# Optimization experiments

Measured on AMD Instinct MI355X. Metric: run time of the kernel, lower is better.

## Reference

```python
import jax, jax.numpy as jnp
from jax import lax
import numpy as np


def conv4d(x, w, b, pad):
    """4D conv (stride 1) as a sum of 3D convs over the first-spatial-dim kernel taps.
    x: [B, Cin, T, D, H, W]; w: [Cout, Cin, Kt, Kd, Kh, Kw]; same pad on all dims."""
    B, Cin, T, D, H, W = x.shape
    Cout, _, Kt = w.shape[:3]
    xp = jnp.pad(x, ((0, 0), (0, 0), (pad, pad), (0, 0), (0, 0), (0, 0)))
    Tout = T + 2 * pad - Kt + 1
    acc = None
    for k in range(Kt):  # loop over kernel taps (<=3), not data dims
        xs = xp[:, :, k:k + Tout]                      # [B,Cin,Tout,D,H,W]
        xs = xs.transpose(0, 2, 1, 3, 4, 5).reshape(B * Tout, Cin, D, H, W)
        y = lax.conv_general_dilated(
            xs, w[:, :, k], (1, 1, 1), [(pad, pad)] * 3,
            dimension_numbers=('NCDHW', 'OIDHW', 'NCDHW'))
        acc = y if acc is None else acc + y
    Do, Ho, Wo = acc.shape[2:]
    out = acc.reshape(B, Tout, Cout, Do, Ho, Wo).transpose(0, 2, 1, 3, 4, 5)
    return out + b[None, :, None, None, None, None]


def tconv4d_k2s2(x, w, b):
    """4D transposed conv, kernel=2, stride=2, pad=0 (non-overlapping blocks).
    x: [B,Cin,T,D,H,W]; w: [Cin,Cout,2,2,2,2] (PyTorch ConvTranspose layout)."""
    B, Cin, T, D, H, W = x.shape
    Cout = w.shape[1]
    y = jnp.einsum('bcijkl,copqrs->boipjqkrls', x, w)
    y = y.reshape(B, Cout, 2 * T, 2 * D, 2 * H, 2 * W)
    return y + b[None, :, None, None, None, None]


def setup_inputs() -> dict:
    key = jax.random.key(0)
    ks = jax.random.split(key, 10)
    Cin, Cout = 64, 32
    x1 = jax.random.normal(ks[0], (2, Cin, 8, 8, 8, 8), dtype=jnp.float32)
    x2 = jax.random.normal(ks[1], (2, Cin // 2, 16, 16, 16, 16), dtype=jnp.float32)
    def w(k, shape, fan_in):
        return jax.random.normal(k, shape, dtype=jnp.float32) / np.float32(np.sqrt(fan_in))
    up_w = w(ks[2], (Cin, Cin // 2, 2, 2, 2, 2), Cin * 16)
    up_b = w(ks[3], (Cin // 2,), Cin * 16)
    w1 = w(ks[4], (Cout, Cin, 3, 3, 3, 3), Cin * 81)
    b1 = w(ks[5], (Cout,), Cin * 81)
    w2 = w(ks[6], (Cout, Cout, 3, 3, 3, 3), Cout * 81)
    b2 = w(ks[7], (Cout,), Cout * 81)
    w3 = w(ks[8], (Cout, Cin, 1, 1, 1, 1), Cin)
    b3 = w(ks[9], (Cout,), Cin)
    return {'x1': x1, 'x2': x2, 'up_w': up_w, 'up_b': up_b,
            'w1': w1, 'b1': b1, 'w2': w2, 'b2': b2, 'w3': w3, 'b3': b3}


def reference(x1, x2, up_w, up_b, w1, b1, w2, b2, w3, b3):
    x1u = tconv4d_k2s2(x1, up_w, up_b)              # [B, Cin//2, 16,16,16,16]
    xc = jnp.concatenate([x2, x1u], axis=1)          # [B, Cin, 16,16,16,16]
    Y = jax.nn.relu(conv4d(xc, w1, b1, 1))
    Y = conv4d(Y, w2, b2, 1)
    sc = conv4d(xc, w3, b3, 0)                       # 1x1 residual projection
    return jax.nn.relu(Y + sc)
```

## Files before the change

### kernel.cpp

```cpp
#include <hip/hip_runtime.h>

typedef unsigned short u16;
typedef __attribute__((ext_vector_type(8))) short short8;
typedef __attribute__((ext_vector_type(4))) float f32x4;

#define XCB_OFF  0
#define Y1B_OFF  8388608
#define W1P_OFF  12582912
#define W2P_OFF  12748800
#define W3P_OFF  12831744
#define UPWP_OFF 12833792
#define X1T_OFF  12866560

__device__ __forceinline__ u16 f2bf(float v) {
    unsigned u = __builtin_bit_cast(unsigned, v);
    u += 0x7FFFu + ((u >> 16) & 1u);
    return (u16)(u >> 16);
}

__device__ __forceinline__ f32x4 MFMA(short8 a, short8 b, f32x4 c) {
    return __builtin_amdgcn_mfma_f32_16x16x32_bf16(a, b, c, 0, 0, 0);
}

__device__ __forceinline__ void decode_bid(int bid, int& b, int& t, int& d, int& h0) {
    int xcd = bid & 7, loc = bid >> 3;
    int hB = loc & 1;
    d = (loc >> 1) & 15;
    int tsub = (loc >> 5) & 1;
    b = loc >> 6;
    t = xcd * 2 + tsub;
    h0 = hB * 8;
}

__global__ __launch_bounds__(256) void setup(const float* __restrict__ w1,
                                             const float* __restrict__ w2,
                                             const float* __restrict__ w3,
                                             const float* __restrict__ upw,
                                             const float* __restrict__ x1,
                                             const float* __restrict__ x2,
                                             u16* __restrict__ ws) {
    __shared__ u16 lds[256 * 66];
    int bid = blockIdx.x;
    int tid = threadIdx.x;
    if (bid < 1108) {
        int idx = bid * 256 + tid;
        if (idx < 165888) {
            int j = idx & 7, lane = (idx >> 3) & 63, rest = idx >> 9;
            int half = rest & 1, chunk = (rest >> 1) & 1, tap = rest >> 2;
            int co = half * 16 + (lane & 15), ci = chunk * 32 + (lane >> 4) * 8 + j;
            ws[W1P_OFF + idx] = f2bf(w1[(co * 64 + ci) * 81 + tap]);
        } else if (idx < 165888 + 82944) {
            int i2 = idx - 165888;
            int j = i2 & 7, lane = (i2 >> 3) & 63, rest = i2 >> 9;
            int half = rest & 1, tap = rest >> 1;
            int co = half * 16 + (lane & 15), ci = (lane >> 4) * 8 + j;
            ws[W2P_OFF + i2] = f2bf(w2[(co * 32 + ci) * 81 + tap]);
        } else if (idx < 165888 + 82944 + 2048) {
            int i3 = idx - (165888 + 82944);
            int j = i3 & 7, lane = (i3 >> 3) & 63, rest = i3 >> 9;
            int half = rest & 1, chunk = rest >> 1;
            int co = half * 16 + (lane & 15), ci = chunk * 32 + (lane >> 4) * 8 + j;
            ws[W3P_OFF + i3] = f2bf(w3[co * 64 + ci]);
        } else if (idx < 250880 + 32768) {
            int i4 = idx - 250880;
            int j = i4 & 7, lane = (i4 >> 3) & 63, rest = i4 >> 9;
            int half = rest & 1, chunk = (rest >> 1) & 1, tap = rest >> 2;
            int co = half * 16 + (lane & 15), ci = chunk * 32 + (lane >> 4) * 8 + j;
            ws[UPWP_OFF + i4] = f2bf(upw[(ci * 32 + co) * 16 + tap]);
        }
    } else if (bid < 1620) {
        int lb = bid - 1108;
        int b = lb >> 8;
        int pos_base = (lb & 255) * 256;
        u16* xcb = ws + XCB_OFF;
        #pragma unroll
        for (int c = 0; c < 32; ++c) {
            lds[tid * 40 + c] = f2bf(x2[((b * 32 + c) << 16) + pos_base + tid]);
        }
        __syncthreads();
        #pragma unroll
        for (int k = 0; k < 4; ++k) {
            int f = k * 256 + tid;
            int u = f & 3, pos = f >> 2;
            uint4 v = *(const uint4*)(lds + pos * 40 + u * 8);
            *(uint4*)(xcb + (size_t)((b << 16) + pos_base + pos) * 64 + u * 8) = v;
        }
    } else {
        int lb = bid - 1620;
        int b = lb >> 4;
        int pos_base = (lb & 15) * 256;
        u16* x1t = ws + X1T_OFF;
        #pragma unroll
        for (int c = 0; c < 64; ++c) {
            lds[tid * 66 + c] = f2bf(x1[((b * 64 + c) << 12) + pos_base + tid]);
        }
        __syncthreads();
        #pragma unroll
        for (int k = 0; k < 64; ++k) {
            int f = k * 256 + tid;
            int ci = f & 63, pos = f >> 6;
            x1t[(size_t)((b << 12) + pos_base + pos) * 64 + ci] = lds[pos * 66 + ci];
        }
    }
}

__global__ __launch_bounds__(256) void xc_up_mfma(const u16* __restrict__ x1t,
                                                  const u16* __restrict__ upwp,
                                                  const float* __restrict__ up_b,
                                                  u16* __restrict__ xcb) {
    int tid = threadIdx.x;
    int wv = tid >> 6, lane = tid & 63;
    int q = lane >> 4, m = lane & 15;
    int wid = blockIdx.x * 4 + wv;
    int j = wid & 63, tap = (wid >> 6) & 15, b = wid >> 10;

    f32x4 acc[4][2];
    {
        float4 bi0 = ((const float4*)up_b)[q];
        float4 bi1 = ((const float4*)up_b)[4 + q];
        #pragma unroll
        for (int g = 0; g < 4; ++g) {
            acc[g][0] = (f32x4){bi0.x, bi0.y, bi0.z, bi0.w};
            acc[g][1] = (f32x4){bi1.x, bi1.y, bi1.z, bi1.w};
        }
    }

    const short8* wv8 = (const short8*)upwp;
    const u16* xb = x1t + (size_t)((b << 12) + (j << 6) + m) * 64;
    #pragma unroll
    for (int chunk = 0; chunk < 2; ++chunk) {
        short8 a0 = wv8[((tap * 2 + chunk) * 2 + 0) * 64 + lane];
        short8 a1 = wv8[((tap * 2 + chunk) * 2 + 1) * 64 + lane];
        #pragma unroll
        for (int g = 0; g < 4; ++g) {
            short8 bf = *(const short8*)(xb + (size_t)(g * 16) * 64 + chunk * 32 + q * 8);
            acc[g][0] = MFMA(a0, bf, acc[g][0]);
            acc[g][1] = MFMA(a1, bf, acc[g][1]);
        }
    }

    int it = j >> 3, id = j & 7;
    int pt = tap >> 3, pd = (tap >> 2) & 1, ph = (tap >> 1) & 1, pw = tap & 1;
    int oT = 2 * it + pt, oD = 2 * id + pd, oW = 2 * (m & 7) + pw;
    #pragma unroll
    for (int g = 0; g < 4; ++g) {
        int ih = g * 2 + (m >> 3);
        int opos = oT * 4096 + oD * 256 + (2 * ih + ph) * 16 + oW;
        u16* op = xcb + (size_t)((b << 16) + opos) * 64 + 32 + q * 4;
        #pragma unroll
        for (int half = 0; half < 2; ++half) {
            f32x4 v = acc[g][half];
            uint2 o;
            o.x = (unsigned)f2bf(v.x) | ((unsigned)f2bf(v.y) << 16);
            o.y = (unsigned)f2bf(v.z) | ((unsigned)f2bf(v.w) << 16);
            *(uint2*)(op + half * 16) = o;
        }
    }
}

__global__ __launch_bounds__(256, 4) void conv1_mfma(const u16* __restrict__ xcb,
                                                     const u16* __restrict__ w1p,
                                                     const float* __restrict__ b1,
                                                     u16* __restrict__ y1b) {
    __shared__ u16 lds[11520];
    int tid = threadIdx.x;
    int lane = tid & 63, wv = tid >> 6;
    int q = lane >> 4, m = lane & 15;
    int c = wv & 1, rg = wv >> 1;
    int b, t, d, h0;
    decode_bid(blockIdx.x, b, t, d, h0);
    int rot = (blockIdx.x * 5) % 9;

    int lofs[6], gofs[6];
    bool st[6], inr[6];
    #pragma unroll
    for (int k = 0; k < 6; ++k) {
        int ui = tid + k * 256;
        int u = ui & 7, p = (ui >> 3) % 18, hh = ui / 144;
        int gh = h0 - 1 + hh, gw = p - 1;
        st[k] = ui < 1440;
        inr[k] = st[k] && ((unsigned)gh < 16u) && ((unsigned)gw < 16u);
        gofs[k] = (gh * 16 + gw) * 64 + u * 8;
        lofs[k] = hh * 1152 + p * 64 + ((u ^ (p & 7)) * 8);
    }

    f32x4 acc[4][2];
    if (c == 0) {
        float4 bi0 = ((const float4*)b1)[q];
        float4 bi1 = ((const float4*)b1)[4 + q];
        #pragma unroll
        for (int i = 0; i < 4; ++i) {
            acc[i][0] = (f32x4){bi0.x, bi0.y, bi0.z, bi0.w};
            acc[i][1] = (f32x4){bi1.x, bi1.y, bi1.z, bi1.w};
        }
    } else {
        #pragma unroll
        for (int i = 0; i < 4; ++i) {
            acc[i][0] = (f32x4){0.f, 0.f, 0.f, 0.f};
            acc[i][1] = (f32x4){0.f, 0.f, 0.f, 0.f};
        }
    }
    const short8* w1v = (const short8*)w1p;

    uint4 rP[6];
    auto load_plane = [&](int ktd) {
        int kt = ktd / 3, kd = ktd - kt * 3;
        int tt = t + kt - 1, dd = d + kd - 1;
        bool pv = ((unsigned)tt < 16u) && ((unsigned)dd < 16u);
        const u16* src = xcb + (size_t)(((b * 16 + tt) * 16 + dd)) * 16384;
        #pragma unroll
        for (int k = 0; k < 6; ++k) {
            uint4 v = {0, 0, 0, 0};
            if (pv && inr[k]) v = *(const uint4*)(src + gofs[k]);
            rP[k] = v;
        }
    };
    auto write_plane = [&]() {
        #pragma unroll
        for (int k = 0; k < 6; ++k)
            if (st[k]) *(uint4*)(lds + lofs[k]) = rP[k];
    };

    load_plane(rot);
    for (int s = 0; s < 9; ++s) {
        int ktd = rot + s; if (ktd >= 9) ktd -= 9;
        __syncthreads();
        write_plane();
        if (s < 8) {
            int nk = ktd + 1; if (nk >= 9) nk -= 9;
            load_plane(nk);
        }
        __syncthreads();
        #pragma unroll
        for (int kw = 0; kw < 3; ++kw) {
            int p = kw + m, pm = p & 7;
            int bo = p * 64 + ((((c << 2) | q) ^ pm) << 3);
            short8 R[6];
            #pragma unroll
            for (int r = 0; r < 6; ++r)
                R[r] = *(const short8*)(lds + (rg * 4 + r) * 1152 + bo);
            #pragma unroll
            for (int kh = 0; kh < 3; ++kh) {
                int tap = (ktd * 3 + kh) * 3 + kw;
                short8 a0 = w1v[((tap * 2 + c) * 2 + 0) * 64 + lane];
                short8 a1 = w1v[((tap * 2 + c) * 2 + 1) * 64 + lane];
                #pragma unroll
                for (int i = 0; i < 4; ++i) {
                    acc[i][0] = MFMA(a0, R[i + kh], acc[i][0]);
                    acc[i][1] = MFMA(a1, R[i + kh], acc[i][1]);
                }
            }
        }
    }

    __syncthreads();
    f32x4* buf = (f32x4*)lds;
    if (c == 1) {
        #pragma unroll
        for (int i = 0; i < 4; ++i)
            #pragma unroll
            for (int half = 0; half < 2; ++half)
                buf[((rg * 4 + i) * 2 + half) * 64 + lane] = acc[i][half];
    }
    __syncthreads();
    if (c == 0) {
        int obase = ((b * 16 + t) * 16 + d) * 256 + (h0 + rg * 4) * 16 + m;
        #pragma unroll
        for (int i = 0; i < 4; ++i) {
            int pos = obase + i * 16;
            #pragma unroll
            for (int half = 0; half < 2; ++half) {
                f32x4 v = acc[i][half];
                f32x4 w = buf[((rg * 4 + i) * 2 + half) * 64 + lane];
                v.x += w.x; v.y += w.y; v.z += w.z; v.w += w.w;
                unsigned r0 = f2bf(fmaxf(v.x, 0.f)), r1 = f2bf(fmaxf(v.y, 0.f));
                unsigned r2 = f2bf(fmaxf(v.z, 0.f)), r3 = f2bf(fmaxf(v.w, 0.f));
                uint2 o;
                o.x = r0 | (r1 << 16);
                o.y = r2 | (r3 << 16);
                *(uint2*)(y1b + (size_t)pos * 32 + half * 16 + q * 4) = o;
            }
        }
    }
}

__global__ __launch_bounds__(256, 4) void conv2_mfma(const u16* __restrict__ y1b,
                                                     const u16* __restrict__ xcb,
                                                     const u16* __restrict__ w2p,
                                                     const u16* __restrict__ w3p,
                                                     const float* __restrict__ b2,
                                                     const float* __restrict__ b3,
                                                     float* __restrict__ out) {
    __shared__ u16 lds[5760];
    int tid = threadIdx.x;
    int lane = tid & 63, wv = tid >> 6;
    int q = lane >> 4, m = lane & 15;
    int hf = wv & 1, rg = wv >> 1;
    int b, t, d, h0;
    decode_bid(blockIdx.x, b, t, d, h0);
    int rot = (blockIdx.x * 5) % 9;

    int lofs[3], gofs[3];
    bool st[3], inr[3];
    #pragma unroll
    for (int k = 0; k < 3; ++k) {
        int ui = tid + k * 256;
        int u = ui & 3, p = (ui >> 2) % 18, hh = ui / 72;
        int gh = h0 - 1 + hh, gw = p - 1;
        st[k] = ui < 720;
        inr[k] = st[k] && ((unsigned)gh < 16u) && ((unsigned)gw < 16u);
        gofs[k] = (gh * 16 + gw) * 32 + u * 8;
        lofs[k] = hh * 576 + p * 32 + ((u ^ (p & 3)) * 8);
    }

    f32x4 acc[4];
    {
        float4 p0 = ((const float4*)b2)[hf * 4 + q];
        float4 s0 = ((const float4*)b3)[hf * 4 + q];
        #pragma unroll
        for (int i = 0; i < 4; ++i)
            acc[i] = (f32x4){p0.x + s0.x, p0.y + s0.y, p0.z + s0.z, p0.w + s0.w};
    }
    const short8* w2v = (const short8*)w2p;

    uint4 rP[3];
    auto load_plane = [&](int ktd) {
        int kt = ktd / 3, kd = ktd - kt * 3;
        int tt = t + kt - 1, dd = d + kd - 1;
        bool pv = ((unsigned)tt < 16u) && ((unsigned)dd < 16u);
        const u16* src = y1b + (size_t)(((b * 16 + tt) * 16 + dd)) * 8192;
        #pragma unroll
        for (int k = 0; k < 3; ++k) {
            uint4 v = {0, 0, 0, 0};
            if (pv && inr[k]) v = *(const uint4*)(src + gofs[k]);
            rP[k] = v;
        }
    };
    auto write_plane = [&]() {
        #pragma unroll
        for (int k = 0; k < 3; ++k)
            if (st[k]) *(uint4*)(lds + lofs[k]) = rP[k];
    };

    load_plane(rot);
    for (int s = 0; s < 9; ++s) {
        int ktd = rot + s; if (ktd >= 9) ktd -= 9;
        __syncthreads();
        write_plane();
        if (s < 8) {
            int nk = ktd + 1; if (nk >= 9) nk -= 9;
            load_plane(nk);
        }
        __syncthreads();
        #pragma unroll
        for (int kw = 0; kw < 3; ++kw) {
            int p = kw + m, pm = p & 3;
            int bo = p * 32 + ((q ^ pm) << 3);
            short8 R[6];
            #pragma unroll
            for (int r = 0; r < 6; ++r)
                R[r] = *(const short8*)(lds + (rg * 4 + r) * 576 + bo);
            #pragma unroll
            for (int kh = 0; kh < 3; ++kh) {
                int tap = (ktd * 3 + kh) * 3 + kw;
                short8 a = w2v[(tap * 2 + hf) * 64 + lane];
                #pragma unroll
                for (int i = 0; i < 4; ++i) {
                    acc[i] = MFMA(a, R[i + kh], acc[i]);
                }
            }
        }
    }

    const short8* w3v = (const short8*)w3p;
    int lpos0 = (t * 16 + d) * 256 + (h0 + rg * 4) * 16 + m;
    int gpos0 = (b << 16) + lpos0;
    #pragma unroll
    for (int chunk = 0; chunk < 2; ++chunk) {
        short8 a = w3v[(chunk * 2 + hf) * 64 + lane];
        #pragma unroll
        for (int i = 0; i < 4; ++i) {
            short8 bf = *(const short8*)(xcb + (size_t)(gpos0 + i * 16) * 64 + ((chunk << 2) | q) * 8);
            acc[i] = MFMA(a, bf, acc[i]);
        }
    }

    #pragma unroll
    for (int i = 0; i < 4; ++i) {
        int lpos = lpos0 + i * 16;
        f32x4 v = acc[i];
        int co = hf * 16 + q * 4;
        float* op = out + (((size_t)(b * 32 + co)) << 16) + lpos;
        op[0ull << 16] = fmaxf(v.x, 0.f);
        op[1ull << 16] = fmaxf(v.y, 0.f);
        op[2ull << 16] = fmaxf(v.z, 0.f);
        op[3ull << 16] = fmaxf(v.w, 0.f);
    }
}

extern "C" void kernel_launch(void* const* d_in, const int* in_sizes, int n_in,
                              void* d_out, int out_size, void* d_ws, size_t ws_size,
                              hipStream_t stream) {
    const float* x1   = (const float*)d_in[0];
    const float* x2   = (const float*)d_in[1];
    const float* up_w = (const float*)d_in[2];
    const float* up_b = (const float*)d_in[3];
    const float* w1   = (const float*)d_in[4];
    const float* b1   = (const float*)d_in[5];
    const float* w2   = (const float*)d_in[6];
    const float* b2   = (const float*)d_in[7];
    const float* w3   = (const float*)d_in[8];
    const float* b3   = (const float*)d_in[9];
    u16* ws  = (u16*)d_ws;
    float* out = (float*)d_out;

    setup<<<1652, 256, 0, stream>>>(w1, w2, w3, up_w, x1, x2, ws);
    xc_up_mfma<<<512, 256, 0, stream>>>(ws + X1T_OFF, ws + UPWP_OFF, up_b, ws + XCB_OFF);
    conv1_mfma<<<1024, 256, 0, stream>>>(ws + XCB_OFF, ws + W1P_OFF, b1, ws + Y1B_OFF);
    conv2_mfma<<<1024, 256, 0, stream>>>(ws + Y1B_OFF, ws + XCB_OFF, ws + W2P_OFF,
                                         ws + W3P_OFF, b2, b3, out);
}
```

Measured before the change: 164.2 us.

## Double-buffer conv2 LDS planes, add MFMA priority hints, vectorize x1 transpose

conv2 now keeps two LDS plane buffers. It writes the next plane after computing on the current one, which drops one barrier per iteration and lets global loads overlap the MFMA work. Both conv kernels raise wave priority with s_setprio around the MFMA loops. The setup kernel's x1 transpose now writes 16-byte vectors instead of scalar u16 stores and is moved to the lowest block ids. The cost is double the LDS in conv2, which may reduce occupancy.

```diff
diff --git a/kernel.cpp b/kernel.cpp
--- a/kernel.cpp
+++ b/kernel.cpp
@@ -39,11 +39,44 @@
                                              const float* __restrict__ x1,
                                              const float* __restrict__ x2,
                                              u16* __restrict__ ws) {
-    __shared__ u16 lds[256 * 66];
+    __shared__ u16 lds[256 * 72];
     int bid = blockIdx.x;
     int tid = threadIdx.x;
-    if (bid < 1108) {
-        int idx = bid * 256 + tid;
+    if (bid < 32) {
+        int b = bid >> 4;
+        int pos_base = (bid & 15) * 256;
+        u16* x1t = ws + X1T_OFF;
+        #pragma unroll
+        for (int c = 0; c < 64; ++c) {
+            lds[tid * 72 + c] = f2bf(x1[((b * 64 + c) << 12) + pos_base + tid]);
+        }
+        __syncthreads();
+        #pragma unroll
+        for (int k = 0; k < 8; ++k) {
+            int f = k * 256 + tid;
+            int u = f & 7, pos = f >> 3;
+            uint4 v = *(const uint4*)(lds + pos * 72 + u * 8);
+            *(uint4*)(x1t + (size_t)((b << 12) + pos_base + pos) * 64 + u * 8) = v;
+        }
+    } else if (bid < 544) {
+        int lb = bid - 32;
+        int b = lb >> 8;
+        int pos_base = (lb & 255) * 256;
+        u16* xcb = ws + XCB_OFF;
+        #pragma unroll
+        for (int c = 0; c < 32; ++c) {
+            lds[tid * 40 + c] = f2bf(x2[((b * 32 + c) << 16) + pos_base + tid]);
+        }
+        __syncthreads();
+        #pragma unroll
+        for (int k = 0; k < 4; ++k) {
+            int f = k * 256 + tid;
+            int u = f & 3, pos = f >> 2;
+            uint4 v = *(const uint4*)(lds + pos * 40 + u * 8);
+            *(uint4*)(xcb + (size_t)((b << 16) + pos_base + pos) * 64 + u * 8) = v;
+        }
+    } else {
+        int idx = (bid - 544) * 256 + tid;
         if (idx < 165888) {
             int j = idx & 7, lane = (idx >> 3) & 63, rest = idx >> 9;
             int half = rest & 1, chunk = (rest >> 1) & 1, tap = rest >> 2;
@@ -68,39 +101,6 @@
             int co = half * 16 + (lane & 15), ci = chunk * 32 + (lane >> 4) * 8 + j;
             ws[UPWP_OFF + i4] = f2bf(upw[(ci * 32 + co) * 16 + tap]);
         }
-    } else if (bid < 1620) {
-        int lb = bid - 1108;
-        int b = lb >> 8;
-        int pos_base = (lb & 255) * 256;
-        u16* xcb = ws + XCB_OFF;
-        #pragma unroll
-        for (int c = 0; c < 32; ++c) {
-            lds[tid * 40 + c] = f2bf(x2[((b * 32 + c) << 16) + pos_base + tid]);
-        }
-        __syncthreads();
-        #pragma unroll
-        for (int k = 0; k < 4; ++k) {
-            int f = k * 256 + tid;
-            int u = f & 3, pos = f >> 2;
-            uint4 v = *(const uint4*)(lds + pos * 40 + u * 8);
-            *(uint4*)(xcb + (size_t)((b << 16) + pos_base + pos) * 64 + u * 8) = v;
-        }
-    } else {
-        int lb = bid - 1620;
-        int b = lb >> 4;
-        int pos_base = (lb & 15) * 256;
-        u16* x1t = ws + X1T_OFF;
-        #pragma unroll
-        for (int c = 0; c < 64; ++c) {
-            lds[tid * 66 + c] = f2bf(x1[((b * 64 + c) << 12) + pos_base + tid]);
-        }
-        __syncthreads();
-        #pragma unroll
-        for (int k = 0; k < 64; ++k) {
-            int f = k * 256 + tid;
-            int ci = f & 63, pos = f >> 6;
-            x1t[(size_t)((b << 12) + pos_base + pos) * 64 + ci] = lds[pos * 66 + ci];
-        }
     }
 }
 
@@ -231,6 +231,7 @@
             load_plane(nk);
         }
         __syncthreads();
+        __builtin_amdgcn_s_setprio(1);
         #pragma unroll
         for (int kw = 0; kw < 3; ++kw) {
             int p = kw + m, pm = p & 7;
@@ -251,6 +252,7 @@
                 }
             }
         }
+        __builtin_amdgcn_s_setprio(0);
     }
 
     __syncthreads();
@@ -291,7 +293,7 @@
                                                      const float* __restrict__ b2,
                                                      const float* __restrict__ b3,
                                                      float* __restrict__ out) {
-    __shared__ u16 lds[5760];
+    __shared__ u16 lds[2][5760];
     int tid = threadIdx.x;
     int lane = tid & 63, wv = tid >> 6;
     int q = lane >> 4, m = lane & 15;
@@ -336,22 +338,21 @@
             rP[k] = v;
         }
     };
-    auto write_plane = [&]() {
+    auto write_plane = [&](int bb) {
         #pragma unroll
         for (int k = 0; k < 3; ++k)
-            if (st[k]) *(uint4*)(lds + lofs[k]) = rP[k];
+            if (st[k]) *(uint4*)(&lds[bb][lofs[k]]) = rP[k];
     };
 
     load_plane(rot);
+    write_plane(0);
+    { int nk = rot + 1; if (nk >= 9) nk -= 9; load_plane(nk); }
+
     for (int s = 0; s < 9; ++s) {
         int ktd = rot + s; if (ktd >= 9) ktd -= 9;
         __syncthreads();
-        write_plane();
-        if (s < 8) {
-            int nk = ktd + 1; if (nk >= 9) nk -= 9;
-            load_plane(nk);
-        }
-        __syncthreads();
+        const u16* L = lds[s & 1];
+        __builtin_amdgcn_s_setprio(1);
         #pragma unroll
         for (int kw = 0; kw < 3; ++kw) {
             int p = kw + m, pm = p & 3;
@@ -359,7 +360,7 @@
             short8 R[6];
             #pragma unroll
             for (int r = 0; r < 6; ++r)
-                R[r] = *(const short8*)(lds + (rg * 4 + r) * 576 + bo);
+                R[r] = *(const short8*)(L + (rg * 4 + r) * 576 + bo);
             #pragma unroll
             for (int kh = 0; kh < 3; ++kh) {
                 int tap = (ktd * 3 + kh) * 3 + kw;
@@ -368,6 +369,14 @@
                 for (int i = 0; i < 4; ++i) {
                     acc[i] = MFMA(a, R[i + kh], acc[i]);
                 }
+            }
+        }
+        __builtin_amdgcn_s_setprio(0);
+        if (s < 8) {
+            write_plane((s + 1) & 1);
+            if (s < 7) {
+                int nk = ktd + 2; if (nk >= 9) nk -= 9;
+                load_plane(nk);
             }
         }
     }
```

Measured after the change: 159.6 us. -2.8%, faster.
